# Kernel optimization log

Measured on AMD Instinct MI355X. Metric: run time of the kernel, lower is better.

Reference implementation:

```python
import jax, jax.numpy as jnp
import numpy as np

WS = 8          # window size
HEADS = 16      # num heads

def conv2d(x, w, padding=0, groups=1):
    return jax.lax.conv_general_dilated(
        x, w, window_strides=(1, 1),
        padding=((padding, padding), (padding, padding)),
        feature_group_count=groups,
        dimension_numbers=('NCHW', 'OIHW', 'NCHW'))

def bn(x, scale, bias):  # inference BN folded into per-channel affine
    return x * scale[None, :, None, None] + bias[None, :, None, None]

def relative_position_index(ws):
    coords = np.stack(np.meshgrid(np.arange(ws), np.arange(ws), indexing='ij'))  # (2, ws, ws)
    cf = coords.reshape(2, -1)
    rc = (cf[:, :, None] - cf[:, None, :]).transpose(1, 2, 0)  # (n, n, 2)
    rc[:, :, 0] += ws - 1
    rc[:, :, 1] += ws - 1
    rc[:, :, 0] *= 2 * ws - 1
    return rc.sum(-1)  # (n, n) int

def avg_pool(x, kh, kw, ph, pw):
    # AvgPool2d with count_include_pad=True (zero pad, divide by full kernel size)
    s = jax.lax.reduce_window(x, 0.0, jax.lax.add, (1, 1, kh, kw), (1, 1, 1, 1),
                              ((0, 0), (0, 0), (ph, ph), (pw, pw)))
    return s / (kh * kw)

def setup_inputs() -> dict:
    key = jax.random.key(0)
    ks = jax.random.split(key, 12)
    C = 256
    x = jax.random.normal(ks[0], (4, C, 128, 128), dtype=jnp.float32)
    inp = {
        'x': x,
        'qkv_w':     jax.random.normal(ks[1], (3 * C, C, 1, 1), jnp.float32) * 0.05,
        'local1_w':  jax.random.normal(ks[2], (C, C, 3, 3), jnp.float32) * 0.05,
        'local1_scale': jnp.ones((C,), jnp.float32),
        'local1_bias':  jnp.zeros((C,), jnp.float32),
        'local2_w':  jax.random.normal(ks[3], (C, C, 1, 1), jnp.float32) * 0.05,
        'local2_scale': jnp.ones((C,), jnp.float32),
        'local2_bias':  jnp.zeros((C,), jnp.float32),
        'dw_w':      jax.random.normal(ks[4], (C, 1, WS, WS), jnp.float32) * 0.05,
        'proj_scale': jnp.ones((C,), jnp.float32),
        'proj_bias':  jnp.zeros((C,), jnp.float32),
        'pw_w':      jax.random.normal(ks[5], (C, C, 1, 1), jnp.float32) * 0.05,
        'rel_bias_table': jax.random.normal(ks[6], ((2 * WS - 1) ** 2, HEADS), jnp.float32) * 0.02,
    }
    return inp

def reference(x, qkv_w, local1_w, local1_scale, local1_bias,
              local2_w, local2_scale, local2_bias,
              dw_w, proj_scale, proj_bias, pw_w, rel_bias_table):
    B, C, H, W = x.shape
    ws, h = WS, HEADS
    d = C // h
    scale = d ** -0.5

    # local branches
    local = bn(conv2d(x, local2_w, padding=0), local2_scale, local2_bias) \
          + bn(conv2d(x, local1_w, padding=1), local1_scale, local1_bias)

    # reflect-pad to multiple of ws (static shapes)
    pad_h = (ws - H % ws) % ws
    pad_w = (ws - W % ws) % ws
    xp = x
    if pad_w:
        xp = jnp.pad(xp, ((0, 0), (0, 0), (0, 0), (0, pad_w)), mode='reflect')
    if pad_h:
        xp = jnp.pad(xp, ((0, 0), (0, 0), (0, pad_h), (0, 0)), mode='reflect')
    Hp, Wp = xp.shape[2], xp.shape[3]
    hh, ww = Hp // ws, Wp // ws

    # qkv: 1x1 conv, then window partition
    qkv = conv2d(xp, qkv_w)  # (B, 3C, Hp, Wp)
    qkv = qkv.reshape(B, 3, h, d, hh, ws, ww, ws)
    qkv = qkv.transpose(1, 0, 4, 6, 2, 5, 7, 3)  # (3, B, hh, ww, h, ws, ws, d)
    qkv = qkv.reshape(3, B * hh * ww, h, ws * ws, d)
    q, k, v = qkv[0], qkv[1], qkv[2]

    dots = jnp.einsum('whid,whjd->whij', q, k) * scale
    rpi = relative_position_index(ws)  # (n, n)
    bias = rel_bias_table[rpi.reshape(-1)].reshape(ws * ws, ws * ws, h)
    dots = dots + bias.transpose(2, 0, 1)[None]
    attn = jax.nn.softmax(dots, axis=-1)
    out = jnp.einsum('whij,whjd->whid', attn, v)

    # windows back to image
    out = out.reshape(B, hh, ww, h, ws, ws, d)
    out = out.transpose(0, 3, 6, 1, 4, 2, 5).reshape(B, C, Hp, Wp)
    out = out[:, :, :H, :W]

    # boundary smoothing avg pools (reflect pad 1 then zero-padded avg pool)
    ax = avg_pool(jnp.pad(out, ((0, 0), (0, 0), (0, 1), (0, 0)), mode='reflect'),
                  ws, 1, ws // 2 - 1, 0)
    ay = avg_pool(jnp.pad(out, ((0, 0), (0, 0), (0, 0), (0, 1)), mode='reflect'),
                  1, ws, 0, ws // 2 - 1)
    out = ax + ay + local

    # pad_out + separable conv projection
    out = jnp.pad(out, ((0, 0), (0, 0), (0, 1), (0, 1)), mode='reflect')
    out = conv2d(out, dw_w, padding=(ws - 1) // 2, groups=C)  # depthwise 8x8
    out = bn(out, proj_scale, proj_bias)
    out = conv2d(out, pw_w)  # pointwise 1x1
    return out[:, :, :H, :W]
```

## Files before the change

kernel.cpp:

```cpp
#include <hip/hip_runtime.h>
#include <cstddef>

#define HH 128
#define WW2 128
#define HWSZ (HH*WW2)
#define CCH 256

typedef __attribute__((ext_vector_type(8))) short short8v;
typedef __attribute__((ext_vector_type(16))) float f32x16;
typedef __attribute__((ext_vector_type(4)))  float f32x4;

__device__ __forceinline__ ushort bf16rte(float v) {
    uint u = __float_as_uint(v);
    uint r = u + 0x7FFFu + ((u >> 16) & 1u);
    return (ushort)(r >> 16);
}

__global__ __launch_bounds__(256) void k_fold(const float* __restrict__ l1w, const float* __restrict__ l1s,
                                              const float* __restrict__ l1b, const float* __restrict__ l2w,
                                              const float* __restrict__ l2s, const float* __restrict__ l2b,
                                              float* __restrict__ Wf, float* __restrict__ biasf) {
    int idx = blockIdx.x * 256 + threadIdx.x;
    if (idx < 2304 * 256) {
        int co = idx & 255;
        int i2 = idx >> 8;
        int ci = i2 / 9;
        int k  = i2 - ci * 9;
        float w = l1s[co] * l1w[co * 2304 + ci * 9 + k];
        if (k == 4) w += l2s[co] * l2w[co * 256 + ci];
        Wf[i2 * 256 + co] = w;
    }
    if (idx < 256) biasf[idx] = l1b[idx] + l2b[idx];
}

__global__ __launch_bounds__(256) void k_wsplit(const float* __restrict__ Wf,
                                                ushort* __restrict__ ahi, ushort* __restrict__ alo) {
    int idx = blockIdx.x * 256 + threadIdx.x;
    if (idx >= 589824) return;
    int j    = idx & 7;
    int lane = (idx >> 3) & 63;
    int t2   = idx >> 9;
    int kb   = t2 % 144;
    int cob  = t2 / 144;
    int cc  = kb / 18; int rem = kb - cc * 18; int tap = rem >> 1; int ks = rem & 1;
    int ci  = cc * 32 + ks * 16 + ((lane >> 5) << 3) + j;
    int co  = cob * 32 + (lane & 31);
    float v = Wf[(size_t)(ci * 9 + tap) * 256 + co];
    ushort h = bf16rte(v);
    float hf = __uint_as_float((uint)h << 16);
    ushort l = bf16rte(v - hf);
    ahi[idx] = h;
    alo[idx] = l;
}

__global__ __launch_bounds__(256) void k_aswz(const float* __restrict__ qkvw,
                                              ushort* __restrict__ aqh, ushort* __restrict__ aql) {
    int idx = blockIdx.x * 256 + threadIdx.x;
    if (idx >= 196608) return;
    int j    = idx & 7;
    int lane = (idx >> 3) & 63;
    int t2   = idx >> 9;
    int kk   = t2 & 7;
    int hp   = t2 >> 3;
    int p    = hp % 3, h = hp / 3;
    int co = p * 256 + h * 16 + (lane & 15);
    int ci = kk * 32 + ((lane >> 4) << 3) + j;
    float v = qkvw[(size_t)co * 256 + ci];
    ushort hi = bf16rte(v);
    float hf = __uint_as_float((uint)hi << 16);
    aqh[idx] = hi;
    aql[idx] = bf16rte(v - hf);
}

__global__ __launch_bounds__(256) void k_cvt(const float* __restrict__ x,
                                             ushort* __restrict__ xhi, ushort* __restrict__ xlo) {
    __shared__ uint pk[32 * 265];
    int t = threadIdx.x;
    int bid = blockIdx.x;
    int b = bid >> 9;
    int px0 = (bid & 511) * 32;
    const float* xb = x + (size_t)b * CCH * HWSZ;
    for (int step = 0; step < 32; ++step) {
        int ci = step * 8 + (t >> 5);
        float v = xb[(size_t)ci * HWSZ + px0 + (t & 31)];
        ushort h = bf16rte(v);
        float hf = __uint_as_float((uint)h << 16);
        ushort l = bf16rte(v - hf);
        pk[(t & 31) * 265 + ci] = ((uint)h << 16) | l;
    }
    __syncthreads();
    int pxl = t >> 3, o = t & 7;
    uint* hp = (uint*)xhi;
    uint* lp = (uint*)xlo;
    size_t pb2 = ((size_t)b * HWSZ + px0 + pxl) * 128;
#pragma unroll
    for (int m = 0; m < 16; ++m) {
        int cip = m * 16 + o * 2;
        uint p0 = pk[pxl * 265 + cip];
        uint p1 = pk[pxl * 265 + cip + 1];
        hp[pb2 + m * 8 + o] = (p1 & 0xFFFF0000u) | (p0 >> 16);
        lp[pb2 + m * 8 + o] = (p1 << 16) | (p0 & 0xFFFFu);
    }
}

__global__ __launch_bounds__(256) void k_conv3m(const ushort* __restrict__ xhi, const ushort* __restrict__ xlo,
                                                const ushort* __restrict__ afr_hi, const ushort* __restrict__ afr_lo,
                                                const float* __restrict__ biasf, float* __restrict__ outp) {
    __shared__ __align__(16) ushort Xsh[12960];
    char* xsb = (char*)Xsh;

    int t = threadIdx.x;
    int bid = blockIdx.x;
    int cb = bid & 1;
    int t2 = bid >> 1;
    int tile_c = t2 & 7;
    int tile_r = (t2 >> 3) & 15;
    int b = t2 >> 7;
    int x0 = tile_c * 16, y0 = tile_r * 8;

    int w = t >> 6, lane = t & 63;
    int co_w = cb * 128 + (w >> 1) * 64;
    int pr0 = (w & 1) * 4;
    int pr_l = (lane & 31) >> 4;
    int pc = lane & 15;
    int kl = lane >> 5;
    int lb0 = (pr0 + 0 + pr_l) * 1296 + pc * 72 + kl * 16;
    int lb1 = (pr0 + 2 + pr_l) * 1296 + pc * 72 + kl * 16;

    const short8v* Ahi = (const short8v*)afr_hi;
    const short8v* Alo = (const short8v*)afr_lo;
    int cobase = (co_w >> 5) * 144 * 64;

    f32x16 c00 = {}, c01 = {}, c10 = {}, c11 = {};

    for (int cc = 0; cc < 8; ++cc) {
        __syncthreads();
#pragma unroll
        for (int it = 0; it < 6; ++it) {
            int i = t + it * 256;
            if (i < 1440) {
                int oct = i & 3;
                int j2 = i >> 2;
                int plane = j2 & 1;
                int loc = j2 >> 1;
                int r = loc / 18, c = loc - r * 18;
                int gy = y0 - 1 + r, gx = x0 - 1 + c;
                uint4 v = make_uint4(0u, 0u, 0u, 0u);
                if (gy >= 0 && gy < 128 && gx >= 0 && gx < 128) {
                    const ushort* src = plane ? xlo : xhi;
                    v = *(const uint4*)(src + ((size_t)(b * HWSZ + gy * 128 + gx) * 256 + cc * 32 + oct * 8));
                }
                *(uint4*)(xsb + plane * 12960 + loc * 72 + oct * 16) = v;
            }
        }
        __syncthreads();

        int baseA = cobase + cc * 18 * 64 + lane;
#pragma unroll
        for (int tap = 0; tap < 9; ++tap) {
            const int ky = tap / 3, kx = tap - ky * 3;
#pragma unroll
            for (int ks = 0; ks < 2; ++ks) {
                const int boff = ky * 1296 + kx * 72 + ks * 32;
                short8v b0h = *(const short8v*)(xsb + lb0 + boff);
                short8v b0l = *(const short8v*)(xsb + lb0 + boff + 12960);
                short8v b1h = *(const short8v*)(xsb + lb1 + boff);
                short8v b1l = *(const short8v*)(xsb + lb1 + boff + 12960);
                int ai = baseA + (tap * 2 + ks) * 64;
                short8v a0h = Ahi[ai];
                short8v a0l = Alo[ai];
                short8v a1h = Ahi[ai + 144 * 64];
                short8v a1l = Alo[ai + 144 * 64];
                c00 = __builtin_amdgcn_mfma_f32_32x32x16_bf16(a0h, b0h, c00, 0, 0, 0);
                c00 = __builtin_amdgcn_mfma_f32_32x32x16_bf16(a0h, b0l, c00, 0, 0, 0);
                c00 = __builtin_amdgcn_mfma_f32_32x32x16_bf16(a0l, b0h, c00, 0, 0, 0);
                c01 = __builtin_amdgcn_mfma_f32_32x32x16_bf16(a0h, b1h, c01, 0, 0, 0);
                c01 = __builtin_amdgcn_mfma_f32_32x32x16_bf16(a0h, b1l, c01, 0, 0, 0);
                c01 = __builtin_amdgcn_mfma_f32_32x32x16_bf16(a0l, b1h, c01, 0, 0, 0);
                c10 = __builtin_amdgcn_mfma_f32_32x32x16_bf16(a1h, b0h, c10, 0, 0, 0);
                c10 = __builtin_amdgcn_mfma_f32_32x32x16_bf16(a1h, b0l, c10, 0, 0, 0);
                c10 = __builtin_amdgcn_mfma_f32_32x32x16_bf16(a1l, b0h, c10, 0, 0, 0);
                c11 = __builtin_amdgcn_mfma_f32_32x32x16_bf16(a1h, b1h, c11, 0, 0, 0);
                c11 = __builtin_amdgcn_mfma_f32_32x32x16_bf16(a1h, b1l, c11, 0, 0, 0);
                c11 = __builtin_amdgcn_mfma_f32_32x32x16_bf16(a1l, b1h, c11, 0, 0, 0);
            }
        }
    }

    int colg = x0 + pc;
    int row0 = y0 + pr0 + pr_l;
    int row1 = row0 + 2;
#pragma unroll
    for (int r = 0; r < 16; ++r) {
        int rr = (r & 3) + 8 * (r >> 2) + 4 * kl;
        {
            int co = co_w + rr;
            float bv = biasf[co];
            float* ob = outp + ((size_t)(b * CCH + co)) * HWSZ;
            ob[row0 * 128 + colg] = c00[r] + bv;
            ob[row1 * 128 + colg] = c01[r] + bv;
        }
        {
            int co = co_w + 32 + rr;
            float bv = biasf[co];
            float* ob = outp + ((size_t)(b * CCH + co)) * HWSZ;
            ob[row0 * 128 + colg] = c10[r] + bv;
            ob[row1 * 128 + colg] = c11[r] + bv;
        }
    }
}

__global__ __launch_bounds__(256, 3) void k_attn(const ushort* __restrict__ xhi, const ushort* __restrict__ xlo,
                                                 const ushort* __restrict__ aqh, const ushort* __restrict__ aql,
                                                 const float* __restrict__ bt, float* __restrict__ attnout) {
    __shared__ float qkvb[2][48 * 64];
    __shared__ float btl[16 * 225];

    int t = threadIdx.x;
    int wv = __builtin_amdgcn_readfirstlane(t >> 6);
    int lane = t & 63;
    int widx = blockIdx.x;
    int b = widx >> 8;
    int rem = widx & 255;
    int hy = rem >> 4, wx = rem & 15;
    int y0 = hy * 8, x0 = wx * 8;

    for (int i = t; i < 3600; i += 256) {
        int rpi = i >> 4, hh = i & 15;
        btl[hh * 225 + rpi] = bt[i];
    }

    int tokb = (wv << 4) | (lane & 15);
    int pixb = (y0 + (tokb >> 3)) * 128 + (x0 + (tokb & 7));
    const ushort* xbh = xhi + ((size_t)b * HWSZ + pixb) * 256 + ((lane >> 4) << 3);
    const ushort* xbl = xlo + ((size_t)b * HWSZ + pixb) * 256 + ((lane >> 4) << 3);
    short8v bh_[8], bl_[8];
#pragma unroll
    for (int kk = 0; kk < 8; ++kk) {
        bh_[kk] = *(const short8v*)(xbh + kk * 32);
        bl_[kk] = *(const short8v*)(xbl + kk * 32);
    }

    const short8v* AhB = (const short8v*)aqh + lane;
    const short8v* AlB = (const short8v*)aql + lane;
    int wrow = ((lane >> 4) << 2);
    int wtok = (wv << 4) + (lane & 15);

    {
#pragma unroll
        for (int p = 0; p < 3; ++p) {
            f32x4 c = {};
#pragma unroll
            for (int kk = 0; kk < 8; ++kk) {
                short8v ah = AhB[(p * 8 + kk) * 64];
                short8v al = AlB[(p * 8 + kk) * 64];
                c = __builtin_amdgcn_mfma_f32_16x16x32_bf16(ah, bh_[kk], c, 0, 0, 0);
                c = __builtin_amdgcn_mfma_f32_16x16x32_bf16(ah, bl_[kk], c, 0, 0, 0);
                c = __builtin_amdgcn_mfma_f32_16x16x32_bf16(al, bh_[kk], c, 0, 0, 0);
            }
            float* bw = &qkvb[0][(p * 16 + wrow) * 64 + wtok];
            bw[0] = c[0]; bw[64] = c[1]; bw[128] = c[2]; bw[192] = c[3];
        }
    }
    __syncthreads();

    int irow = wv * 16 + (lane & 15);
    int jg = lane >> 4;
    int iy = irow >> 3, ix = irow & 7;

#pragma unroll 2
    for (int h = 0; h < 16; ++h) {
        int h2 = (h + 1) & 15;
        int nb = (h + 1) & 1;
        const short8v* Ah = AhB + (size_t)h2 * 24 * 64;
        const short8v* Al = AlB + (size_t)h2 * 24 * 64;
#pragma unroll
        for (int p = 0; p < 3; ++p) {
            f32x4 c = {};
#pragma unroll
            for (int kk = 0; kk < 8; ++kk) {
                short8v ah = Ah[(p * 8 + kk) * 64];
                short8v al = Al[(p * 8 + kk) * 64];
                c = __builtin_amdgcn_mfma_f32_16x16x32_bf16(ah, bh_[kk], c, 0, 0, 0);
                c = __builtin_amdgcn_mfma_f32_16x16x32_bf16(ah, bl_[kk], c, 0, 0, 0);
                c = __builtin_amdgcn_mfma_f32_16x16x32_bf16(al, bh_[kk], c, 0, 0, 0);
            }
            float* bw = &qkvb[nb][(p * 16 + wrow) * 64 + wtok];
            bw[0] = c[0]; bw[64] = c[1]; bw[128] = c[2]; bw[192] = c[3];
        }

        const float* buf = qkvb[h & 1];
        float qd[16];
#pragma unroll
        for (int d = 0; d < 16; ++d) qd[d] = buf[d * 64 + irow];
        float s[16];
#pragma unroll
        for (int jj = 0; jj < 16; ++jj) s[jj] = 0.f;
#pragma unroll
        for (int d = 0; d < 16; ++d) {
            const float* kp = &buf[(16 + d) * 64 + jg * 16];
#pragma unroll
            for (int m = 0; m < 4; ++m) {
                float4 kv = *(const float4*)(kp + m * 4);
                s[m * 4 + 0] += qd[d] * kv.x;
                s[m * 4 + 1] += qd[d] * kv.y;
                s[m * 4 + 2] += qd[d] * kv.z;
                s[m * 4 + 3] += qd[d] * kv.w;
            }
        }
#pragma unroll
        for (int jj = 0; jj < 16; ++jj) {
            int j = jg * 16 + jj;
            int jy = j >> 3, jx = j & 7;
            int rpi = (iy - jy + 7) * 15 + (ix - jx + 7);
            s[jj] = s[jj] * 0.25f + btl[h * 225 + rpi];
        }
        float mx = s[0];
#pragma unroll
        for (int jj = 1; jj < 16; ++jj) mx = fmaxf(mx, s[jj]);
        mx = fmaxf(mx, __shfl_xor(mx, 16));
        mx = fmaxf(mx, __shfl_xor(mx, 32));
        float ls = 0.f;
#pragma unroll
        for (int jj = 0; jj < 16; ++jj) { s[jj] = __expf(s[jj] - mx); ls += s[jj]; }
        ls += __shfl_xor(ls, 16);
        ls += __shfl_xor(ls, 32);
        float inv = 1.0f / ls;
#pragma unroll
        for (int d = 0; d < 16; ++d) {
            const float* vp = &buf[(32 + d) * 64 + jg * 16];
            float o0 = 0.f, o1 = 0.f;
#pragma unroll
            for (int m = 0; m < 4; ++m) {
                float4 vvv = *(const float4*)(vp + m * 4);
                o0 += s[m * 4 + 0] * vvv.x + s[m * 4 + 1] * vvv.y;
                o1 += s[m * 4 + 2] * vvv.z + s[m * 4 + 3] * vvv.w;
            }
            float o = o0 + o1;
            o += __shfl_xor(o, 16);
            o += __shfl_xor(o, 32);
            if (jg == 0)
                attnout[((size_t)(b * CCH + h * 16 + d)) * HWSZ + (y0 + iy) * 128 + (x0 + ix)] = o * inv;
        }
        __syncthreads();
    }
}

__global__ __launch_bounds__(256) void k_pools(const float* __restrict__ attnout, const float* __restrict__ localb,
                                               float* __restrict__ sbuf) {
    for (int i = blockIdx.x * 256 + threadIdx.x; i < 4 * CCH * HWSZ; i += gridDim.x * 256) {
        int xc = i & 127;
        int y  = (i >> 7) & 127;
        int bc = i >> 14;
        const float* pl = attnout + (size_t)bc * HWSZ;
        float axs = 0.f;
#pragma unroll
        for (int d = -3; d <= 4; ++d) {
            int t2 = y + d;
            if (t2 >= 0 && t2 < 128) axs += pl[t2 * 128 + xc];
        }
        if (y >= 124) axs += pl[126 * 128 + xc];
        float ays = 0.f;
#pragma unroll
        for (int d = -3; d <= 4; ++d) {
            int t2 = xc + d;
            if (t2 >= 0 && t2 < 128) ays += pl[y * 128 + t2];
        }
        if (xc >= 124) ays += pl[y * 128 + 126];
        sbuf[i] = (axs + ays) * 0.125f + localb[i];
    }
}

__device__ __forceinline__ void dw_loadrow(const float* __restrict__ sp, int trow, int j, float* dst) {
    if (trow < 0 || trow > 128) {
#pragma unroll
        for (int q = 0; q < 8; ++q) dst[q] = 0.f;
        return;
    }
    int sr = (trow == 128) ? 126 : trow;
    const float* rp = sp + sr * 128;
#pragma unroll
    for (int q = 0; q < 8; ++q) {
        int col = j - 3 + q;
        float v = 0.f;
        if (col >= 0 && col <= 128) v = rp[(col == 128) ? 126 : col];
        dst[q] = v;
    }
}

__global__ __launch_bounds__(256) void k_dw(const float* __restrict__ sbuf, const float* __restrict__ dww,
                                            const float* __restrict__ pscale, const float* __restrict__ pbias,
                                            float* __restrict__ tbuf) {
    int t = threadIdx.x;
    int j = t & 127;
    int half = __builtin_amdgcn_readfirstlane(t >> 7);
    int bid = blockIdx.x;
    int c = (bid & 127) * 2 + half;
    int b = bid >> 7;
    const float* sp = sbuf + ((size_t)(b * CCH + c)) * HWSZ;
    float wloc[64];
    const float* dwp = dww + c * 64;
#pragma unroll
    for (int i = 0; i < 64; ++i) wloc[i] = dwp[i];
    float scale = pscale[c], bias = pbias[c];

    float rbuf[8][8];
#pragma unroll
    for (int tr = -3; tr <= 4; ++tr) {
        dw_loadrow(sp, tr, j, rbuf[(tr + 8) & 7]);
    }
    float* op = tbuf + ((size_t)(b * CCH + c)) * HWSZ;
    for (int yb = 0; yb < 16; ++yb) {
#pragma unroll
        for (int k = 0; k < 8; ++k) {
            int y = yb * 8 + k;
            float a0 = 0.f, a1 = 0.f, a2 = 0.f, a3 = 0.f;
#pragma unroll
            for (int p = 0; p < 8; ++p) {
                const int slot = (k + 5 + p) & 7;
                float part = 0.f;
#pragma unroll
                for (int q = 0; q < 8; ++q) part += wloc[p * 8 + q] * rbuf[slot][q];
                if ((p & 3) == 0) a0 += part;
                else if ((p & 3) == 1) a1 += part;
                else if ((p & 3) == 2) a2 += part;
                else a3 += part;
            }
            op[y * 128 + j] = scale * ((a0 + a1) + (a2 + a3)) + bias;
            dw_loadrow(sp, y + 5, j, rbuf[(k + 5) & 7]);
        }
    }
}

__global__ __launch_bounds__(256) void k_pw(const float* __restrict__ tbuf, const float* __restrict__ pww,
                                            float* __restrict__ outp) {
    __shared__ __align__(16) float xs[8][128];
    __shared__ __align__(16) float wsm[8][64];
    int t = threadIdx.x;
    int bid = blockIdx.x;
    int cb = bid & 3;
    int row = bid >> 2;
    int y = row & 127;
    int b = row >> 7;
    int cg = t >> 4;
    int px = (t & 15) * 8;
    float acc[4][8];
#pragma unroll
    for (int c = 0; c < 4; ++c)
#pragma unroll
        for (int j = 0; j < 8; ++j) acc[c][j] = 0.f;
    const float* tb = tbuf + (size_t)b * CCH * HWSZ + y * 128;

    for (int cc = 0; cc < 32; ++cc) {
        __syncthreads();
        {
            int i = t;
#pragma unroll
            for (int it = 0; it < 4; ++it, i += 256) {
                int ci = i >> 7, p = i & 127;
                xs[ci][p] = tb[(size_t)(cc * 8 + ci) * HWSZ + p];
            }
        }
        for (int i = t; i < 512; i += 256) {
            int ci = i >> 6, co = i & 63;
            wsm[ci][co] = pww[(size_t)(cb * 64 + co) * 256 + cc * 8 + ci];
        }
        __syncthreads();
#pragma unroll
        for (int ci = 0; ci < 8; ++ci) {
            float4 w = *(const float4*)&wsm[ci][cg * 4];
            float4 xa = *(const float4*)&xs[ci][px];
            float4 xbv = *(const float4*)&xs[ci][px + 4];
            float xf[8] = {xa.x, xa.y, xa.z, xa.w, xbv.x, xbv.y, xbv.z, xbv.w};
#pragma unroll
            for (int j = 0; j < 8; ++j) {
                acc[0][j] += w.x * xf[j];
                acc[1][j] += w.y * xf[j];
                acc[2][j] += w.z * xf[j];
                acc[3][j] += w.w * xf[j];
            }
        }
    }
#pragma unroll
    for (int c = 0; c < 4; ++c) {
        int co = cb * 64 + cg * 4 + c;
        float* op = outp + ((size_t)(b * CCH + co)) * HWSZ + y * 128 + px;
        *(float4*)op = make_float4(acc[c][0], acc[c][1], acc[c][2], acc[c][3]);
        *(float4*)(op + 4) = make_float4(acc[c][4], acc[c][5], acc[c][6], acc[c][7]);
    }
}

extern "C" void kernel_launch(void* const* d_in, const int* in_sizes, int n_in,
                              void* d_out, int out_size, void* d_ws, size_t ws_size,
                              hipStream_t stream) {
    const float* x    = (const float*)d_in[0];
    const float* qkvw = (const float*)d_in[1];
    const float* l1w  = (const float*)d_in[2];
    const float* l1s  = (const float*)d_in[3];
    const float* l1b  = (const float*)d_in[4];
    const float* l2w  = (const float*)d_in[5];
    const float* l2s  = (const float*)d_in[6];
    const float* l2b  = (const float*)d_in[7];
    const float* dww  = (const float*)d_in[8];
    const float* ps   = (const float*)d_in[9];
    const float* pb   = (const float*)d_in[10];
    const float* pww  = (const float*)d_in[11];
    const float* bt   = (const float*)d_in[12];
    float* out = (float*)d_out;
    float* wsf = (float*)d_ws;

    const size_t nWf = 589824;
    const size_t nPlane = 16777216;
    const size_t nAq = 196608;
    size_t need = (nWf + 256 + 3 * nPlane) * sizeof(float) + (2 * 589824 + 2 * nAq) * sizeof(ushort);
    if (ws_size < need) return;

    float* Wf      = wsf;
    float* biasf   = wsf + nWf;
    float* attnout = wsf + nWf + 256;
    float* localb  = attnout + nPlane;
    float* sbuf    = localb + nPlane;
    float* tbuf    = attnout;
    ushort* xhi = (ushort*)sbuf;
    ushort* xlo = xhi + nPlane;
    ushort* ahi = (ushort*)(sbuf + nPlane);
    ushort* alo = ahi + 589824;
    ushort* aqh = alo + 589824;
    ushort* aql = aqh + nAq;

    k_fold  <<<2304, 256, 0, stream>>>(l1w, l1s, l1b, l2w, l2s, l2b, Wf, biasf);
    k_wsplit<<<2304, 256, 0, stream>>>(Wf, ahi, alo);
    k_aswz  <<<768,  256, 0, stream>>>(qkvw, aqh, aql);
    k_cvt   <<<2048, 256, 0, stream>>>(x, xhi, xlo);
    k_conv3m<<<1024, 256, 0, stream>>>(xhi, xlo, ahi, alo, biasf, localb);
    k_attn  <<<1024, 256, 0, stream>>>(xhi, xlo, aqh, aql, bt, attnout);
    k_pools <<<4096, 256, 0, stream>>>(attnout, localb, sbuf);
    k_dw    <<<512,  256, 0, stream>>>(sbuf, dww, ps, pb, tbuf);
    k_pw    <<<2048, 256, 0, stream>>>(tbuf, pww, out);
}
```

Measured before the change: 884.2 us.

## Move pointwise conv to split-bf16 MFMA and retile 3x3 conv for occupancy

Replaces the FP32 FMA pointwise 1x1 conv with an MFMA kernel. The new kernel splits activations into bf16 hi/lo parts in shared memory and reads weights prepared by a new swizzle kernel. The 3x3 local conv now uses half as many output channels per block, doubles the grid, remaps block order, and asks the launch bounds for three blocks per CU. The aim is higher occupancy and tensor-core throughput, at the cost of reloading each input tile twice as often and one extra small prep launch.

```diff
diff --git a/kernel.cpp b/kernel.cpp
--- a/kernel.cpp
+++ b/kernel.cpp
@@ -72,6 +72,24 @@
     aql[idx] = bf16rte(v - hf);
 }
 
+__global__ __launch_bounds__(256) void k_pswz(const float* __restrict__ pww,
+                                              ushort* __restrict__ apwh, ushort* __restrict__ apwl) {
+    int idx = blockIdx.x * 256 + threadIdx.x;
+    if (idx >= 65536) return;
+    int j    = idx & 7;
+    int lane = (idx >> 3) & 63;
+    int t2   = idx >> 9;
+    int ks   = t2 & 15;
+    int cob  = t2 >> 4;
+    int co = cob * 32 + (lane & 31);
+    int ci = ks * 16 + ((lane >> 5) << 3) + j;
+    float v = pww[(size_t)co * 256 + ci];
+    ushort h = bf16rte(v);
+    float hf = __uint_as_float((uint)h << 16);
+    apwh[idx] = h;
+    apwl[idx] = bf16rte(v - hf);
+}
+
 __global__ __launch_bounds__(256) void k_cvt(const float* __restrict__ x,
                                              ushort* __restrict__ xhi, ushort* __restrict__ xlo) {
     __shared__ uint pk[32 * 265];
@@ -103,35 +121,36 @@
     }
 }
 
-__global__ __launch_bounds__(256) void k_conv3m(const ushort* __restrict__ xhi, const ushort* __restrict__ xlo,
-                                                const ushort* __restrict__ afr_hi, const ushort* __restrict__ afr_lo,
-                                                const float* __restrict__ biasf, float* __restrict__ outp) {
+__global__ __launch_bounds__(256, 3) void k_conv3m(const ushort* __restrict__ xhi, const ushort* __restrict__ xlo,
+                                                   const ushort* __restrict__ afr_hi, const ushort* __restrict__ afr_lo,
+                                                   const float* __restrict__ biasf, float* __restrict__ outp) {
     __shared__ __align__(16) ushort Xsh[12960];
     char* xsb = (char*)Xsh;
 
     int t = threadIdx.x;
-    int bid = blockIdx.x;
-    int cb = bid & 1;
-    int t2 = bid >> 1;
+    int orig = blockIdx.x;
+    int bid = (orig & 7) * 256 + (orig >> 3);
+    int cb = bid & 3;
+    int t2 = bid >> 2;
     int tile_c = t2 & 7;
     int tile_r = (t2 >> 3) & 15;
     int b = t2 >> 7;
     int x0 = tile_c * 16, y0 = tile_r * 8;
 
     int w = t >> 6, lane = t & 63;
-    int co_w = cb * 128 + (w >> 1) * 64;
-    int pr0 = (w & 1) * 4;
+    int cs = w & 1, ph = w >> 1;
+    int co_w = cb * 64 + cs * 32;
     int pr_l = (lane & 31) >> 4;
     int pc = lane & 15;
     int kl = lane >> 5;
-    int lb0 = (pr0 + 0 + pr_l) * 1296 + pc * 72 + kl * 16;
-    int lb1 = (pr0 + 2 + pr_l) * 1296 + pc * 72 + kl * 16;
+    int lb0 = (ph * 4 + pr_l) * 1296 + pc * 72 + kl * 16;
+    int lb1 = lb0 + 2 * 1296;
 
     const short8v* Ahi = (const short8v*)afr_hi;
     const short8v* Alo = (const short8v*)afr_lo;
-    int cobase = (co_w >> 5) * 144 * 64;
-
-    f32x16 c00 = {}, c01 = {}, c10 = {}, c11 = {};
+    int cobase = (cb * 2 + cs) * 144 * 64;
+
+    f32x16 c0 = {}, c1 = {};
 
     for (int cc = 0; cc < 8; ++cc) {
         __syncthreads();
@@ -167,46 +186,29 @@
                 short8v b1h = *(const short8v*)(xsb + lb1 + boff);
                 short8v b1l = *(const short8v*)(xsb + lb1 + boff + 12960);
                 int ai = baseA + (tap * 2 + ks) * 64;
-                short8v a0h = Ahi[ai];
-                short8v a0l = Alo[ai];
-                short8v a1h = Ahi[ai + 144 * 64];
-                short8v a1l = Alo[ai + 144 * 64];
-                c00 = __builtin_amdgcn_mfma_f32_32x32x16_bf16(a0h, b0h, c00, 0, 0, 0);
-                c00 = __builtin_amdgcn_mfma_f32_32x32x16_bf16(a0h, b0l, c00, 0, 0, 0);
-                c00 = __builtin_amdgcn_mfma_f32_32x32x16_bf16(a0l, b0h, c00, 0, 0, 0);
-                c01 = __builtin_amdgcn_mfma_f32_32x32x16_bf16(a0h, b1h, c01, 0, 0, 0);
-                c01 = __builtin_amdgcn_mfma_f32_32x32x16_bf16(a0h, b1l, c01, 0, 0, 0);
-                c01 = __builtin_amdgcn_mfma_f32_32x32x16_bf16(a0l, b1h, c01, 0, 0, 0);
-                c10 = __builtin_amdgcn_mfma_f32_32x32x16_bf16(a1h, b0h, c10, 0, 0, 0);
-                c10 = __builtin_amdgcn_mfma_f32_32x32x16_bf16(a1h, b0l, c10, 0, 0, 0);
-                c10 = __builtin_amdgcn_mfma_f32_32x32x16_bf16(a1l, b0h, c10, 0, 0, 0);
-                c11 = __builtin_amdgcn_mfma_f32_32x32x16_bf16(a1h, b1h, c11, 0, 0, 0);
-                c11 = __builtin_amdgcn_mfma_f32_32x32x16_bf16(a1h, b1l, c11, 0, 0, 0);
-                c11 = __builtin_amdgcn_mfma_f32_32x32x16_bf16(a1l, b1h, c11, 0, 0, 0);
+                short8v ah = Ahi[ai];
+                short8v al = Alo[ai];
+                c0 = __builtin_amdgcn_mfma_f32_32x32x16_bf16(ah, b0h, c0, 0, 0, 0);
+                c0 = __builtin_amdgcn_mfma_f32_32x32x16_bf16(ah, b0l, c0, 0, 0, 0);
+                c0 = __builtin_amdgcn_mfma_f32_32x32x16_bf16(al, b0h, c0, 0, 0, 0);
+                c1 = __builtin_amdgcn_mfma_f32_32x32x16_bf16(ah, b1h, c1, 0, 0, 0);
+                c1 = __builtin_amdgcn_mfma_f32_32x32x16_bf16(ah, b1l, c1, 0, 0, 0);
+                c1 = __builtin_amdgcn_mfma_f32_32x32x16_bf16(al, b1h, c1, 0, 0, 0);
             }
         }
     }
 
     int colg = x0 + pc;
-    int row0 = y0 + pr0 + pr_l;
+    int row0 = y0 + ph * 4 + pr_l;
     int row1 = row0 + 2;
 #pragma unroll
     for (int r = 0; r < 16; ++r) {
         int rr = (r & 3) + 8 * (r >> 2) + 4 * kl;
-        {
-            int co = co_w + rr;
-            float bv = biasf[co];
-            float* ob = outp + ((size_t)(b * CCH + co)) * HWSZ;
-            ob[row0 * 128 + colg] = c00[r] + bv;
-            ob[row1 * 128 + colg] = c01[r] + bv;
-        }
-        {
-            int co = co_w + 32 + rr;
-            float bv = biasf[co];
-            float* ob = outp + ((size_t)(b * CCH + co)) * HWSZ;
-            ob[row0 * 128 + colg] = c10[r] + bv;
-            ob[row1 * 128 + colg] = c11[r] + bv;
-        }
+        int co = co_w + rr;
+        float bv = biasf[co];
+        float* ob = outp + ((size_t)(b * CCH + co)) * HWSZ;
+        ob[row0 * 128 + colg] = c0[r] + bv;
+        ob[row1 * 128 + colg] = c1[r] + bv;
     }
 }
 
@@ -432,61 +434,64 @@
     }
 }
 
-__global__ __launch_bounds__(256) void k_pw(const float* __restrict__ tbuf, const float* __restrict__ pww,
-                                            float* __restrict__ outp) {
-    __shared__ __align__(16) float xs[8][128];
-    __shared__ __align__(16) float wsm[8][64];
+__global__ __launch_bounds__(256) void k_pwm(const float* __restrict__ tbuf,
+                                             const ushort* __restrict__ apwh, const ushort* __restrict__ apwl,
+                                             float* __restrict__ outp) {
+    __shared__ __align__(16) ushort pBh[32][264];
+    __shared__ __align__(16) ushort pBl[32][264];
+
     int t = threadIdx.x;
     int bid = blockIdx.x;
-    int cb = bid & 3;
-    int row = bid >> 2;
-    int y = row & 127;
-    int b = row >> 7;
-    int cg = t >> 4;
-    int px = (t & 15) * 8;
-    float acc[4][8];
-#pragma unroll
-    for (int c = 0; c < 4; ++c)
-#pragma unroll
-        for (int j = 0; j < 8; ++j) acc[c][j] = 0.f;
-    const float* tb = tbuf + (size_t)b * CCH * HWSZ + y * 128;
-
-    for (int cc = 0; cc < 32; ++cc) {
-        __syncthreads();
+    int b = bid >> 9;
+    int px0 = (bid & 511) * 32;
+    int px = t & 31;
+
+    for (int it = 0; it < 32; ++it) {
+        int ci = it * 8 + (t >> 5);
+        float v = tbuf[((size_t)(b * CCH + ci)) * HWSZ + px0 + px];
+        ushort h = bf16rte(v);
+        float hf = __uint_as_float((uint)h << 16);
+        pBh[px][ci] = h;
+        pBl[px][ci] = bf16rte(v - hf);
+    }
+    __syncthreads();
+
+    int w = t >> 6, lane = t & 63;
+    int kl = lane >> 5;
+    int pc = lane & 31;
+    const short8v* Ah = (const short8v*)apwh;
+    const short8v* Al = (const short8v*)apwl;
+    int a0base = ((w * 2) * 16) * 64 + lane;
+    int a1base = ((w * 2 + 1) * 16) * 64 + lane;
+
+    f32x16 c0 = {}, c1 = {};
+#pragma unroll
+    for (int ks = 0; ks < 16; ++ks) {
+        short8v bh = *(const short8v*)&pBh[pc][ks * 16 + kl * 8];
+        short8v bl = *(const short8v*)&pBl[pc][ks * 16 + kl * 8];
+        short8v a0h = Ah[a0base + ks * 64];
+        short8v a0l = Al[a0base + ks * 64];
+        short8v a1h = Ah[a1base + ks * 64];
+        short8v a1l = Al[a1base + ks * 64];
+        c0 = __builtin_amdgcn_mfma_f32_32x32x16_bf16(a0h, bh, c0, 0, 0, 0);
+        c0 = __builtin_amdgcn_mfma_f32_32x32x16_bf16(a0h, bl, c0, 0, 0, 0);
+        c0 = __builtin_amdgcn_mfma_f32_32x32x16_bf16(a0l, bh, c0, 0, 0, 0);
+        c1 = __builtin_amdgcn_mfma_f32_32x32x16_bf16(a1h, bh, c1, 0, 0, 0);
+        c1 = __builtin_amdgcn_mfma_f32_32x32x16_bf16(a1h, bl, c1, 0, 0, 0);
+        c1 = __builtin_amdgcn_mfma_f32_32x32x16_bf16(a1l, bh, c1, 0, 0, 0);
+    }
+
+#pragma unroll
+    for (int r = 0; r < 16; ++r) {
+        int rr = (r & 3) + 8 * (r >> 2) + 4 * kl;
         {
-            int i = t;
-#pragma unroll
-            for (int it = 0; it < 4; ++it, i += 256) {
-                int ci = i >> 7, p = i & 127;
-                xs[ci][p] = tb[(size_t)(cc * 8 + ci) * HWSZ + p];
-            }
-        }
-        for (int i = t; i < 512; i += 256) {
-            int ci = i >> 6, co = i & 63;
-            wsm[ci][co] = pww[(size_t)(cb * 64 + co) * 256 + cc * 8 + ci];
-        }
-        __syncthreads();
-#pragma unroll
-        for (int ci = 0; ci < 8; ++ci) {
-            float4 w = *(const float4*)&wsm[ci][cg * 4];
-            float4 xa = *(const float4*)&xs[ci][px];
-            float4 xbv = *(const float4*)&xs[ci][px + 4];
-            float xf[8] = {xa.x, xa.y, xa.z, xa.w, xbv.x, xbv.y, xbv.z, xbv.w};
-#pragma unroll
-            for (int j = 0; j < 8; ++j) {
-                acc[0][j] += w.x * xf[j];
-                acc[1][j] += w.y * xf[j];
-                acc[2][j] += w.z * xf[j];
-                acc[3][j] += w.w * xf[j];
-            }
-        }
-    }
-#pragma unroll
-    for (int c = 0; c < 4; ++c) {
-        int co = cb * 64 + cg * 4 + c;
-        float* op = outp + ((size_t)(b * CCH + co)) * HWSZ + y * 128 + px;
-        *(float4*)op = make_float4(acc[c][0], acc[c][1], acc[c][2], acc[c][3]);
-        *(float4*)(op + 4) = make_float4(acc[c][4], acc[c][5], acc[c][6], acc[c][7]);
+            int co = w * 64 + rr;
+            outp[((size_t)(b * CCH + co)) * HWSZ + px0 + pc] = c0[r];
+        }
+        {
+            int co = w * 64 + 32 + rr;
+            outp[((size_t)(b * CCH + co)) * HWSZ + px0 + pc] = c1[r];
+        }
     }
 }
 
@@ -512,7 +517,9 @@
     const size_t nWf = 589824;
     const size_t nPlane = 16777216;
     const size_t nAq = 196608;
-    size_t need = (nWf + 256 + 3 * nPlane) * sizeof(float) + (2 * 589824 + 2 * nAq) * sizeof(ushort);
+    const size_t nApw = 65536;
+    size_t need = (nWf + 256 + 3 * nPlane) * sizeof(float)
+                + (2 * 589824 + 2 * nAq + 2 * nApw) * sizeof(ushort);
     if (ws_size < need) return;
 
     float* Wf      = wsf;
@@ -527,14 +534,17 @@
     ushort* alo = ahi + 589824;
     ushort* aqh = alo + 589824;
     ushort* aql = aqh + nAq;
+    ushort* apwh = aql + nAq;
+    ushort* apwl = apwh + nApw;
 
     k_fold  <<<2304, 256, 0, stream>>>(l1w, l1s, l1b, l2w, l2s, l2b, Wf, biasf);
     k_wsplit<<<2304, 256, 0, stream>>>(Wf, ahi, alo);
     k_aswz  <<<768,  256, 0, stream>>>(qkvw, aqh, aql);
+    k_pswz  <<<256,  256, 0, stream>>>(pww, apwh, apwl);
     k_cvt   <<<2048, 256, 0, stream>>>(x, xhi, xlo);
-    k_conv3m<<<1024, 256, 0, stream>>>(xhi, xlo, ahi, alo, biasf, localb);
+    k_conv3m<<<2048, 256, 0, stream>>>(xhi, xlo, ahi, alo, biasf, localb);
     k_attn  <<<1024, 256, 0, stream>>>(xhi, xlo, aqh, aql, bt, attnout);
     k_pools <<<4096, 256, 0, stream>>>(attnout, localb, sbuf);
     k_dw    <<<512,  256, 0, stream>>>(sbuf, dww, ps, pb, tbuf);
-    k_pw    <<<2048, 256, 0, stream>>>(tbuf, pww, out);
-}
+    k_pwm   <<<2048, 256, 0, stream>>>(tbuf, apwh, apwl, out);
+}
```

Measured after the change: 996.4 us. 1.13x slower.
